# Performance work log

Measured on AMD Instinct MI355X. Metric: run time of the kernel, lower is better.

Reference implementation:

```python
import jax, jax.numpy as jnp
import numpy as np

# --- hash-grid / Field hyperparams (from init_kwargs defaults) ---
L = 16            # n_levels
F = 2             # n_features_per_level
LOG2_T = 19
T = 1 << LOG2_T   # hashmap size per level
NMIN = 16         # base_resolution
MAXRES = 512
SCALE = 1.0
HIDDEN = 32
OUT_DIM = 1
N = 2_000_000
B = float(np.exp(np.log(MAXRES * SCALE / NMIN) / (L - 1)))  # per_level_scale
PRIMES = jnp.array([1, 2654435761, 805459861], dtype=jnp.uint32)
# 8 corner offsets of the unit cube, (8,3)
CORNERS = jnp.array([[(c >> 0) & 1, (c >> 1) & 1, (c >> 2) & 1] for c in range(8)], dtype=jnp.uint32)


def hash_encode(xn, table):
    """xn: (N,3) in [0,1]; table: (L,T,F). Returns (N, L*F)."""
    feats = []
    for l in range(L):  # fixed small loop over levels
        s = NMIN * (B ** l) - 1.0          # tcnn-style grid scale
        pos = xn * s                        # (N,3)
        p0 = jnp.floor(pos)
        w = pos - p0                        # trilinear fracs, (N,3)
        p0i = p0.astype(jnp.uint32)
        corner = p0i[:, None, :] + CORNERS[None, :, :]          # (N,8,3)
        h = corner * PRIMES                                      # (N,8,3) uint32 wrap-mul
        idx = (h[..., 0] ^ h[..., 1] ^ h[..., 2]) & jnp.uint32(T - 1)  # (N,8)
        # trilinear weights per corner: prod over dims of w or (1-w)
        cw = jnp.where(CORNERS[None, :, :] == 1, w[:, None, :], 1.0 - w[:, None, :])
        cw = cw.prod(axis=-1)                                    # (N,8)
        g = table[l][idx.astype(jnp.int32)]                      # (N,8,F)
        feats.append(jnp.einsum('ncf,nc->nf', g, cw))            # (N,F)
    return jnp.concatenate(feats, axis=-1)                       # (N, L*F)


def setup_inputs() -> dict:
    key = jax.random.key(0)
    ks = jax.random.split(key, 8)
    x = jax.random.uniform(ks[0], (N, 3), jnp.float32)  # coords in [0,1) subset of [-scale,scale]
    table = jax.random.normal(ks[1], (L, T, F), jnp.float32) * 1e-2
    W0 = jax.random.normal(ks[2], (L * F + 3, HIDDEN), jnp.float32) * 0.1
    b0 = jnp.zeros((HIDDEN,), jnp.float32)
    W1 = jax.random.normal(ks[3], (HIDDEN, HIDDEN), jnp.float32) * 0.1
    b1 = jnp.zeros((HIDDEN,), jnp.float32)
    Wout = jax.random.normal(ks[4], (HIDDEN, OUT_DIM), jnp.float32) * 0.1
    bout = jnp.zeros((OUT_DIM,), jnp.float32)
    return {"x": x, "table": table, "W0": W0, "b0": b0, "W1": W1, "b1": b1, "Wout": Wout, "bout": bout}


def reference(x, table, W0, b0, W1, b1, Wout, bout):
    # density(): normalize coords to [0,1]
    xn = (x + SCALE) / (2.0 * SCALE)
    # back_prop=0: encoder sees detached coords
    h = hash_encode(jax.lax.stop_gradient(xn), table)   # (N, L*F)
    feat = jnp.concatenate([xn, h], axis=-1)            # (N, 35)  torch.cat([x, h], 1)
    h1 = jax.nn.elu(feat @ W0 + b0)
    h2 = jax.nn.elu(h1 @ W1 + b1)
    out = h2 @ Wout + bout                              # (N, 1)
    return out
```

## Files before the change

kernel.cpp:

```cpp
#include <hip/hip_runtime.h>
#include <hip/hip_fp16.h>
#include <cmath>

#define LVL   16
#define NDENSE 11
#define NHASH  (LVL - NDENSE)
#define TSIZE (1u << 19)
#define TMASK (TSIZE - 1u)
#define HID   32
#define PRIME1 2654435761u
#define PRIME2 805459861u

struct Scales { float s[LVL]; };
struct DenseInfo {
    int X0[NDENSE];
    int dim[NDENSE];
    int dimsq[NDENSE];
    int base[NDENSE];
    int eoff[NDENSE + 1];
};
struct PtInfo {
    int P1[NDENSE];
    int pbase[NDENSE];
    int ptotal;
};

typedef _Float16 f16x8 __attribute__((ext_vector_type(8)));
typedef float    f32x4 __attribute__((ext_vector_type(4)));
typedef float    f32x2 __attribute__((ext_vector_type(2)));
typedef unsigned u32x4 __attribute__((ext_vector_type(4)));

__device__ __forceinline__ float elu_f(float v) {
    return v > 0.0f ? v : __expf(v) - 1.0f;
}
__device__ __forceinline__ unsigned hashed(unsigned cx, unsigned cy, unsigned cz) {
    return (cx ^ (cy * PRIME1) ^ (cz * PRIME2)) & TMASK;
}

__device__ __forceinline__ unsigned enc_pair(float a, float b) {
    return ((unsigned)__builtin_amdgcn_cvt_pk_fp8_f32(a * 64.0f, b * 64.0f, 0, false)) & 0xFFFFu;
}
__device__ __forceinline__ f32x2 dec_lo(unsigned d) {
    return __builtin_amdgcn_cvt_pk_f32_fp8((int)d, false);
}
__device__ __forceinline__ f32x2 dec_hi(unsigned d) {
    return __builtin_amdgcn_cvt_pk_f32_fp8((int)d, true);
}
__device__ __forceinline__ unsigned pack_ff(_Float16 a, _Float16 b) {
    unsigned short ua = __builtin_bit_cast(unsigned short, a);
    unsigned short ub = __builtin_bit_cast(unsigned short, b);
    return (unsigned)ua | ((unsigned)ub << 16);
}
__device__ __forceinline__ unsigned pack_f2(f32x2 f) {
    return pack_ff((_Float16)f.x, (_Float16)f.y);
}

__global__ __launch_bounds__(256)
void convert_hash8(const f32x2* __restrict__ src, unsigned short* __restrict__ dst)
{
    int i = blockIdx.x * blockDim.x + threadIdx.x;
    if (i >= NHASH * (int)TSIZE) return;
    int l = NDENSE + i / (int)TSIZE;
    int s = i & (int)TMASK;
    f32x2 v = src[(size_t)l * TSIZE + s];
    dst[i] = (unsigned short)enc_pair(v.x, v.y);
}

__global__ __launch_bounds__(256)
void dense_pts(const float* __restrict__ table, unsigned short* __restrict__ pts,
               DenseInfo di, PtInfo pi)
{
    int p = blockIdx.x * blockDim.x + threadIdx.x;
    if (p >= pi.ptotal) return;
    int l = 0;
#pragma unroll
    for (int k = 1; k < NDENSE; ++k) if (p >= pi.pbase[k]) l = k;
    int X0 = 0, D1 = 1, pb = 0;
#pragma unroll
    for (int k = 0; k < NDENSE; ++k)
        if (l == k) { X0 = di.X0[k]; D1 = pi.P1[k]; pb = pi.pbase[k]; }
    int lp = p - pb;
    int x = lp % D1; int r = lp / D1;
    int y = r % D1;  int z = r / D1;
    unsigned cx = (unsigned)(X0 + x), cy = (unsigned)(X0 + y), cz = (unsigned)(X0 + z);
    const f32x2* __restrict__ tl = (const f32x2*)table + (size_t)l * TSIZE;
    f32x2 v = tl[hashed(cx, cy, cz)];
    pts[p] = (unsigned short)enc_pair(v.x, v.y);
}

__global__ __launch_bounds__(256)
void dense_cells(const unsigned short* __restrict__ pts, u32x4* __restrict__ dtab,
                 DenseInfo di, PtInfo pi)
{
    int e = blockIdx.x * blockDim.x + threadIdx.x;
    if (e >= di.eoff[NDENSE]) return;
    int l = 0;
#pragma unroll
    for (int k = 1; k < NDENSE; ++k) if (e >= di.eoff[k]) l = k;
    int D = 1, D1 = 1, base = 0, eo = 0, pb = 0;
#pragma unroll
    for (int k = 0; k < NDENSE; ++k)
        if (l == k) { D = di.dim[k]; D1 = pi.P1[k]; base = di.base[k]; eo = di.eoff[k]; pb = pi.pbase[k]; }
    int le = e - eo;
    int ex = le % D; int r = le / D;
    int ey = r % D;  int ez = r / D;
    const unsigned short* __restrict__ q = pts + pb;
    int i00 = ex + (ey + ez * D1) * D1;
    int i01 = i00 + D1;
    int i10 = i00 + D1 * D1;
    int i11 = i10 + D1;
    u32x4 Q;
    Q.x = (unsigned)q[i00] | ((unsigned)q[i00 + 1] << 16);
    Q.y = (unsigned)q[i01] | ((unsigned)q[i01 + 1] << 16);
    Q.z = (unsigned)q[i10] | ((unsigned)q[i10 + 1] << 16);
    Q.w = (unsigned)q[i11] | ((unsigned)q[i11 + 1] << 16);
    dtab[base + le] = Q;
}

__global__ __launch_bounds__(256)
void dense_prep8(const float* __restrict__ table, u32x4* __restrict__ dtab,
                 DenseInfo di)
{
    int e = blockIdx.x * blockDim.x + threadIdx.x;
    if (e >= di.eoff[NDENSE]) return;
    int l = 0;
#pragma unroll
    for (int k = 1; k < NDENSE; ++k) if (e >= di.eoff[k]) l = k;
    int X0 = 0, D = 1, base = 0, eo = 0;
#pragma unroll
    for (int k = 0; k < NDENSE; ++k)
        if (l == k) { X0 = di.X0[k]; D = di.dim[k]; base = di.base[k]; eo = di.eoff[k]; }
    int le = e - eo;
    int ex = le % D; int r = le / D;
    int ey = r % D;  int ez = r / D;
    unsigned cx = (unsigned)(X0 + ex);
    unsigned cy = (unsigned)(X0 + ey);
    unsigned cz = (unsigned)(X0 + ez);
    const f32x2* __restrict__ tl = (const f32x2*)table + (size_t)l * TSIZE;
    f32x2 c0 = tl[hashed(cx,      cy,      cz)];
    f32x2 c1 = tl[hashed(cx + 1u, cy,      cz)];
    f32x2 c2 = tl[hashed(cx,      cy + 1u, cz)];
    f32x2 c3 = tl[hashed(cx + 1u, cy + 1u, cz)];
    f32x2 c4 = tl[hashed(cx,      cy,      cz + 1u)];
    f32x2 c5 = tl[hashed(cx + 1u, cy,      cz + 1u)];
    f32x2 c6 = tl[hashed(cx,      cy + 1u, cz + 1u)];
    f32x2 c7 = tl[hashed(cx + 1u, cy + 1u, cz + 1u)];
    u32x4 Q;
    Q.x = enc_pair(c0.x, c0.y) | (enc_pair(c1.x, c1.y) << 16);
    Q.y = enc_pair(c2.x, c2.y) | (enc_pair(c3.x, c3.y) << 16);
    Q.z = enc_pair(c4.x, c4.y) | (enc_pair(c5.x, c5.y) << 16);
    Q.w = enc_pair(c6.x, c6.y) | (enc_pair(c7.x, c7.y) << 16);
    dtab[base + le] = Q;
}

__global__ void prep_frags(const float* __restrict__ W0, const float* __restrict__ W1,
                           const float* __restrict__ Wout, _Float16* __restrict__ frags)
{
    int idx = blockIdx.x * blockDim.x + threadIdx.x;
    if (idx >= 14*64*8) return;
    int f = idx >> 9;
    int rem = idx & 511;
    int lane = rem >> 3;
    int j = rem & 7;
    int q = lane >> 4;
    int nn = lane & 15;

    float w = 0.0f;
    bool lo;
    if (f < 8) {
        int part = f >> 2, kt = (f >> 1) & 1, nt = f & 1;
        int k = kt*32 + q*8 + j;
        int ncol = nt*16 + nn;
        float val = 0.0f;
        if (k < 32)      val = W0[(3 + k)  * HID + ncol];
        else if (k < 35) val = W0[(k - 32) * HID + ncol];
        else if (k < 38) val = W0[(k - 35) * HID + ncol];
        w = val; lo = (part == 1);
    } else if (f < 12) {
        int part = (f - 8) >> 1, nt = (f - 8) & 1;
        int k = q*8 + j;
        int ncol = nt*16 + nn;
        w = W1[k * HID + ncol]; lo = (part == 1);
    } else {
        int part = f - 12;
        int k = q*8 + j;
        w = (nn == 0) ? Wout[k] : 0.0f; lo = (part == 1);
    }
    _Float16 hi = (_Float16)w;
    frags[idx] = lo ? (_Float16)(w - (float)hi) : hi;
}

struct HL {
    unsigned d0, d1, d2, d3;
    unsigned e0, e1, e2, e3;
    unsigned i0, i1, i2, i3, dm;
    float wx, wy, wz;
};

__device__ __forceinline__ void hash_issue(HL& h, const unsigned* __restrict__ hq,
                                           float xn0, float xn1, float xn2, float s)
{
    float px = xn0 * s, py = xn1 * s, pz = xn2 * s;
    float fx = floorf(px), fy = floorf(py), fz = floorf(pz);
    h.wx = px - fx; h.wy = py - fy; h.wz = pz - fz;
    unsigned x0 = (unsigned)fx, y0 = (unsigned)fy, z0 = (unsigned)fz;
    unsigned hy0 = y0 * PRIME1, hy1 = hy0 + PRIME1;
    unsigned hz0 = z0 * PRIME2, hz1 = hz0 + PRIME2;
    unsigned b00 = hy0 ^ hz0, b10 = hy1 ^ hz0, b01 = hy0 ^ hz1, b11 = hy1 ^ hz1;
    h.i0 = (x0 ^ b00) & TMASK;
    h.i1 = (x0 ^ b10) & TMASK;
    h.i2 = (x0 ^ b01) & TMASK;
    h.i3 = (x0 ^ b11) & TMASK;
    h.dm = (x0 ^ (x0 + 1u)) & TMASK;
    h.d0 = hq[h.i0 >> 1]; h.d1 = hq[h.i1 >> 1];
    h.d2 = hq[h.i2 >> 1]; h.d3 = hq[h.i3 >> 1];
    unsigned j0 = h.i0 ^ h.dm, j1 = h.i1 ^ h.dm, j2 = h.i2 ^ h.dm, j3 = h.i3 ^ h.dm;
    h.e0 = hq[j0 >> 1]; h.e1 = hq[j1 >> 1];
    h.e2 = hq[j2 >> 1]; h.e3 = hq[j3 >> 1];
}

__device__ __forceinline__ unsigned pick_hw(unsigned d, unsigned idx) {
    return (idx & 1u) ? (d >> 16) : (d & 0xFFFFu);
}

__device__ __forceinline__ f32x2 hash_consume(const HL& h)
{
    f32x2 A0 = dec_lo(pick_hw(h.d0, h.i0)), A1 = dec_lo(pick_hw(h.d1, h.i1));
    f32x2 A2 = dec_lo(pick_hw(h.d2, h.i2)), A3 = dec_lo(pick_hw(h.d3, h.i3));
    unsigned j0 = h.i0 ^ h.dm, j1 = h.i1 ^ h.dm, j2 = h.i2 ^ h.dm, j3 = h.i3 ^ h.dm;
    f32x2 C0 = dec_lo(pick_hw(h.e0, j0)), C1 = dec_lo(pick_hw(h.e1, j1));
    f32x2 C2 = dec_lo(pick_hw(h.e2, j2)), C3 = dec_lo(pick_hw(h.e3, j3));
    float uy  = 1.0f - h.wy;
    float uzs = (1.0f - h.wz) * 0.015625f;
    float wzs = h.wz * 0.015625f;
    float w00 = uy * uzs, w10 = h.wy * uzs, w01 = uy * wzs, w11 = h.wy * wzs;
    f32x2 a = A0 * w00 + A1 * w10 + A2 * w01 + A3 * w11;
    f32x2 c = C0 * w00 + C1 * w10 + C2 * w01 + C3 * w11;
    return a * (1.0f - h.wx) + c * h.wx;
}

__global__ __launch_bounds__(256, 4)
void fused_mfma_kernel(const float* __restrict__ x, const unsigned* __restrict__ htab,
                       const u32x4* __restrict__ dtab,
                       const float* __restrict__ b0, const float* __restrict__ b1,
                       const float* __restrict__ bout, const _Float16* __restrict__ fragbuf,
                       float* __restrict__ out, int n, Scales sc, DenseInfo di)
{
    __shared__ __attribute__((aligned(16))) _Float16 featL[256 * 64];
    __shared__ __attribute__((aligned(16))) _Float16 h1h[4][16*32], h1l[4][16*32];

    const int t = threadIdx.x;
    const int pbase = blockIdx.x * 256;
    const int p  = pbase + t;
    const int pc = p < n ? p : n - 1;

    const float xn0 = (x[3*pc+0] + 1.0f) * 0.5f;
    const float xn1 = (x[3*pc+1] + 1.0f) * 0.5f;
    const float xn2 = (x[3*pc+2] + 1.0f) * 0.5f;

    u32x4 qd[NDENSE];
#pragma unroll
    for (int l = 0; l < NDENSE; ++l) {
        const float s = sc.s[l];
        int D = di.dim[l];
        int cx = (int)floorf(xn0 * s) - di.X0[l];
        int cy = (int)floorf(xn1 * s) - di.X0[l];
        int cz = (int)floorf(xn2 * s) - di.X0[l];
        cx = min(max(cx, 0), D - 1);
        cy = min(max(cy, 0), D - 1);
        cz = min(max(cz, 0), D - 1);
        qd[l] = dtab[(size_t)(di.base[l] + cx + cy * D + cz * di.dimsq[l])];
    }

    HL hA, hB, hC;
    hash_issue(hA, htab + 0 * (TSIZE / 2), xn0, xn1, xn2, sc.s[11]);
    hash_issue(hB, htab + 1 * (TSIZE / 2), xn0, xn1, xn2, sc.s[12]);
    hash_issue(hC, htab + 2 * (TSIZE / 2), xn0, xn1, xn2, sc.s[13]);

    unsigned rr[LVL];

#pragma unroll
    for (int l = 0; l < NDENSE; ++l) {
        const float s = sc.s[l];
        float px = xn0 * s, py = xn1 * s, pz = xn2 * s;
        float wx = px - floorf(px), wy = py - floorf(py), wz = pz - floorf(pz);
        u32x4 Q = qd[l];
        f32x2 a00 = dec_lo(Q.x), a10 = dec_hi(Q.x);
        f32x2 a01 = dec_lo(Q.y), a11 = dec_hi(Q.y);
        f32x2 c00 = dec_lo(Q.z), c10 = dec_hi(Q.z);
        f32x2 c01 = dec_lo(Q.w), c11 = dec_hi(Q.w);
        float ux = 1.0f - wx, uy = 1.0f - wy;
        float uzs = (1.0f - wz) * 0.015625f, wzs = wz * 0.015625f;
        f32x2 t0 = a00 * ux + a10 * wx;
        f32x2 t1 = a01 * ux + a11 * wx;
        f32x2 t2 = c00 * ux + c10 * wx;
        f32x2 t3 = c01 * ux + c11 * wx;
        f32x2 u0 = t0 * uy + t1 * wy;
        f32x2 u1 = t2 * uy + t3 * wy;
        f32x2 f  = u0 * uzs + u1 * wzs;
        rr[l] = pack_f2(f);
    }

    rr[11] = pack_f2(hash_consume(hA));
    hash_issue(hA, htab + 3 * (TSIZE / 2), xn0, xn1, xn2, sc.s[14]);
    rr[12] = pack_f2(hash_consume(hB));
    hash_issue(hB, htab + 4 * (TSIZE / 2), xn0, xn1, xn2, sc.s[15]);
    rr[13] = pack_f2(hash_consume(hC));
    rr[14] = pack_f2(hash_consume(hA));
    rr[15] = pack_f2(hash_consume(hB));

    {
        u32x4* fl = (u32x4*)&featL[t * 64];
        const int swt = t & 7;
        u32x4 ch;
        ch.x = rr[0];  ch.y = rr[1];  ch.z = rr[2];  ch.w = rr[3];  fl[0 ^ swt] = ch;
        ch.x = rr[4];  ch.y = rr[5];  ch.z = rr[6];  ch.w = rr[7];  fl[1 ^ swt] = ch;
        ch.x = rr[8];  ch.y = rr[9];  ch.z = rr[10]; ch.w = rr[11]; fl[2 ^ swt] = ch;
        ch.x = rr[12]; ch.y = rr[13]; ch.z = rr[14]; ch.w = rr[15]; fl[3 ^ swt] = ch;
        _Float16 X0h = (_Float16)xn0, X1h = (_Float16)xn1, X2h = (_Float16)xn2;
        _Float16 L0h = (_Float16)(xn0 - (float)X0h);
        _Float16 L1h = (_Float16)(xn1 - (float)X1h);
        _Float16 L2h = (_Float16)(xn2 - (float)X2h);
        ch.x = pack_ff(X0h, X1h); ch.y = pack_ff(X2h, L0h);
        ch.z = pack_ff(L1h, L2h); ch.w = 0;
        fl[4 ^ swt] = ch;
        u32x4 Z; Z.x = 0; Z.y = 0; Z.z = 0; Z.w = 0;
        fl[5 ^ swt] = Z; fl[6 ^ swt] = Z; fl[7 ^ swt] = Z;
    }

    const int lane = t & 63, w = t >> 6;
    const int q = lane >> 4, nn = lane & 15;

    const f16x8* FB = (const f16x8*)fragbuf;
    f16x8 B0h00 = FB[0*64 + lane], B0h01 = FB[1*64 + lane];
    f16x8 B0h10 = FB[2*64 + lane], B0h11 = FB[3*64 + lane];
    f16x8 B0l00 = FB[4*64 + lane], B0l01 = FB[5*64 + lane];
    f16x8 B0l10 = FB[6*64 + lane], B0l11 = FB[7*64 + lane];
    f16x8 B1h0  = FB[8*64 + lane], B1h1  = FB[9*64 + lane];
    f16x8 B1l0  = FB[10*64 + lane], B1l1 = FB[11*64 + lane];
    f16x8 B2h   = FB[12*64 + lane], B2l  = FB[13*64 + lane];

    float bias00 = b0[nn], bias01 = b0[16 + nn];
    float bias10 = b1[nn], bias11 = b1[16 + nn];
    float biasO  = (nn == 0) ? bout[0] : 0.0f;

    _Float16* H1h = &h1h[w][0]; _Float16* H1l = &h1l[w][0];

#pragma unroll
    for (int mt = 0; mt < 4; ++mt) {
        const int mrow = w*64 + mt*16 + nn;
        const f16x8* ar = (const f16x8*)&featL[mrow * 64];
        f16x8 A0 = ar[q ^ (nn & 7)];
        f16x8 A1 = ar[(4 + q) ^ (nn & 7)];

        f32x4 c0 = {bias00, bias00, bias00, bias00};
        f32x4 c1 = {bias01, bias01, bias01, bias01};
        c0 = __builtin_amdgcn_mfma_f32_16x16x32_f16(A0, B0h00, c0, 0, 0, 0);
        c0 = __builtin_amdgcn_mfma_f32_16x16x32_f16(A1, B0h10, c0, 0, 0, 0);
        c0 = __builtin_amdgcn_mfma_f32_16x16x32_f16(A0, B0l00, c0, 0, 0, 0);
        c0 = __builtin_amdgcn_mfma_f32_16x16x32_f16(A1, B0l10, c0, 0, 0, 0);
        c1 = __builtin_amdgcn_mfma_f32_16x16x32_f16(A0, B0h01, c1, 0, 0, 0);
        c1 = __builtin_amdgcn_mfma_f32_16x16x32_f16(A1, B0h11, c1, 0, 0, 0);
        c1 = __builtin_amdgcn_mfma_f32_16x16x32_f16(A0, B0l01, c1, 0, 0, 0);
        c1 = __builtin_amdgcn_mfma_f32_16x16x32_f16(A1, B0l11, c1, 0, 0, 0);

#pragma unroll
        for (int r = 0; r < 4; ++r) {
            int m = q*4 + r;
            float e0 = elu_f(c0[r]);
            _Float16 hh = (_Float16)e0;
            H1h[m*32 + nn]      = hh;
            H1l[m*32 + nn]      = (_Float16)(e0 - (float)hh);
            float e1 = elu_f(c1[r]);
            hh = (_Float16)e1;
            H1h[m*32 + 16 + nn] = hh;
            H1l[m*32 + 16 + nn] = (_Float16)(e1 - (float)hh);
        }

        f16x8 Ah = *(const f16x8*)(H1h + nn*32 + q*8);
        f16x8 Al = *(const f16x8*)(H1l + nn*32 + q*8);
        f32x4 d0 = {bias10, bias10, bias10, bias10};
        f32x4 d1 = {bias11, bias11, bias11, bias11};
        d0 = __builtin_amdgcn_mfma_f32_16x16x32_f16(Ah, B1h0, d0, 0, 0, 0);
        d0 = __builtin_amdgcn_mfma_f32_16x16x32_f16(Ah, B1l0, d0, 0, 0, 0);
        d0 = __builtin_amdgcn_mfma_f32_16x16x32_f16(Al, B1h0, d0, 0, 0, 0);
        d1 = __builtin_amdgcn_mfma_f32_16x16x32_f16(Ah, B1h1, d1, 0, 0, 0);
        d1 = __builtin_amdgcn_mfma_f32_16x16x32_f16(Ah, B1l1, d1, 0, 0, 0);
        d1 = __builtin_amdgcn_mfma_f32_16x16x32_f16(Al, B1h1, d1, 0, 0, 0);

#pragma unroll
        for (int r = 0; r < 4; ++r) {
            int m = q*4 + r;
            float e0 = elu_f(d0[r]);
            _Float16 hh = (_Float16)e0;
            H1h[m*32 + nn]      = hh;
            H1l[m*32 + nn]      = (_Float16)(e0 - (float)hh);
            float e1 = elu_f(d1[r]);
            hh = (_Float16)e1;
            H1h[m*32 + 16 + nn] = hh;
            H1l[m*32 + 16 + nn] = (_Float16)(e1 - (float)hh);
        }

        f16x8 A2h = *(const f16x8*)(H1h + nn*32 + q*8);
        f16x8 A2l = *(const f16x8*)(H1l + nn*32 + q*8);
        f32x4 c3 = {biasO, biasO, biasO, biasO};
        c3 = __builtin_amdgcn_mfma_f32_16x16x32_f16(A2h, B2h, c3, 0, 0, 0);
        c3 = __builtin_amdgcn_mfma_f32_16x16x32_f16(A2h, B2l, c3, 0, 0, 0);
        c3 = __builtin_amdgcn_mfma_f32_16x16x32_f16(A2l, B2h, c3, 0, 0, 0);

        if (nn == 0) {
            int pout = pbase + w*64 + mt*16 + q*4;
#pragma unroll
            for (int r = 0; r < 4; ++r)
                if (pout + r < n) out[pout + r] = c3[r];
        }
    }
}

__device__ __forceinline__ float2 enc_level_f32(float xn0, float xn1, float xn2, float s,
                                                const float2* __restrict__ tb)
{
    float px = xn0 * s, py = xn1 * s, pz = xn2 * s;
    float fx = floorf(px), fy = floorf(py), fz = floorf(pz);
    float wx = px - fx, wy = py - fy, wz = pz - fz;
    unsigned x0 = (unsigned)fx, y0 = (unsigned)fy, z0 = (unsigned)fz;
    unsigned hy0 = y0 * PRIME1, hy1 = hy0 + PRIME1;
    unsigned hz0 = z0 * PRIME2, hz1 = hz0 + PRIME2;
    unsigned b00 = hy0 ^ hz0, b10 = hy1 ^ hz0, b01 = hy0 ^ hz1, b11 = hy1 ^ hz1;
    float2 g000 = tb[( x0       ^ b00) & TMASK];
    float2 g100 = tb[((x0 + 1u) ^ b00) & TMASK];
    float2 g010 = tb[( x0       ^ b10) & TMASK];
    float2 g110 = tb[((x0 + 1u) ^ b10) & TMASK];
    float2 g001 = tb[( x0       ^ b01) & TMASK];
    float2 g101 = tb[((x0 + 1u) ^ b01) & TMASK];
    float2 g011 = tb[( x0       ^ b11) & TMASK];
    float2 g111 = tb[((x0 + 1u) ^ b11) & TMASK];
    float ux = 1.0f - wx, uy = 1.0f - wy, uz = 1.0f - wz;
    float c00 = uy*uz, c10 = wy*uz, c01 = uy*wz, c11 = wy*wz;
    float f0 = ux * (c00*g000.x + c10*g010.x + c01*g001.x + c11*g011.x)
             + wx * (c00*g100.x + c10*g110.x + c01*g101.x + c11*g111.x);
    float f1 = ux * (c00*g000.y + c10*g010.y + c01*g001.y + c11*g011.y)
             + wx * (c00*g100.y + c10*g110.y + c01*g101.y + c11*g111.y);
    return make_float2(f0, f1);
}

__global__ __launch_bounds__(256, 4)
void fused_fp32_kernel(const float* __restrict__ x, const float* __restrict__ table,
                       const float* __restrict__ W0, const float* __restrict__ b0,
                       const float* __restrict__ W1, const float* __restrict__ b1,
                       const float* __restrict__ Wout, const float* __restrict__ bout,
                       float* __restrict__ out, int n, Scales sc)
{
    int tid = blockIdx.x * blockDim.x + threadIdx.x;
    if (tid >= n) return;
    float xn0 = (x[3*tid+0] + 1.0f) * 0.5f;
    float xn1 = (x[3*tid+1] + 1.0f) * 0.5f;
    float xn2 = (x[3*tid+2] + 1.0f) * 0.5f;
    float acc[HID];
#pragma unroll
    for (int j = 0; j < HID; ++j)
        acc[j] = b0[j] + xn0 * W0[0*HID + j] + xn1 * W0[1*HID + j] + xn2 * W0[2*HID + j];
#pragma unroll
    for (int lv = 0; lv < LVL; ++lv) {
        const float2* tb = (const float2*)table + (size_t)lv * TSIZE;
        float2 f = enc_level_f32(xn0, xn1, xn2, sc.s[lv], tb);
        const float* w0r0 = W0 + (3 + 2*lv) * HID;
        const float* w0r1 = W0 + (4 + 2*lv) * HID;
#pragma unroll
        for (int j = 0; j < HID; ++j)
            acc[j] += f.x * w0r0[j] + f.y * w0r1[j];
    }
#pragma unroll
    for (int j = 0; j < HID; ++j) acc[j] = elu_f(acc[j]);
    float acc2[HID];
#pragma unroll
    for (int j = 0; j < HID; ++j) acc2[j] = b1[j];
#pragma unroll
    for (int k = 0; k < HID; ++k) {
        float hk = acc[k];
        const float* w1r = W1 + k * HID;
#pragma unroll
        for (int j = 0; j < HID; ++j) acc2[j] += hk * w1r[j];
    }
    float o = bout[0];
#pragma unroll
    for (int k = 0; k < HID; ++k) o += elu_f(acc2[k]) * Wout[k];
    out[tid] = o;
}

extern "C" void kernel_launch(void* const* d_in, const int* in_sizes, int n_in,
                              void* d_out, int out_size, void* d_ws, size_t ws_size,
                              hipStream_t stream)
{
    const float* x    = (const float*)d_in[0];
    const float* tb   = (const float*)d_in[1];
    const float* W0   = (const float*)d_in[2];
    const float* b0   = (const float*)d_in[3];
    const float* W1   = (const float*)d_in[4];
    const float* b1   = (const float*)d_in[5];
    const float* Wout = (const float*)d_in[6];
    const float* bo   = (const float*)d_in[7];
    float* out = (float*)d_out;

    int n = in_sizes[0] / 3;

    Scales sc;
    DenseInfo di;
    PtInfo pi;
    double B = exp(log(32.0) / 15.0);
    {
        int base = 0, ecum = 0, pcum = 0;
        for (int l = 0; l < LVL; ++l) {
            double sd = 16.0 * pow(B, (double)l) - 1.0;
            sc.s[l] = (float)sd;
            if (l < NDENSE) {
                int X0   = (int)floor(0.5 * sd) - 2; if (X0 < 0) X0 = 0;
                int Xmax = (int)ceil(sd) + 2;
                int dim  = Xmax - X0 + 1;
                di.X0[l] = X0; di.dim[l] = dim; di.dimsq[l] = dim * dim;
                di.base[l] = base; di.eoff[l] = ecum;
                base += dim * dim * dim;
                ecum += dim * dim * dim;
                int D1 = dim + 1;
                pi.P1[l] = D1; pi.pbase[l] = pcum;
                pcum += D1 * D1 * D1;
            }
        }
        di.eoff[NDENSE] = ecum;
        pi.ptotal = pcum;
    }

    const size_t dense_bytes = (size_t)di.eoff[NDENSE] * 16;
    const size_t hash8_bytes = (size_t)NHASH * TSIZE * 2;
    const size_t frag_bytes  = 14 * 64 * 8 * sizeof(_Float16);
    int block = 256;
    int pgrid = (n + block - 1) / block;

    if (ws_size >= dense_bytes + hash8_bytes + frag_bytes) {
        u32x4*          dtab  = (u32x4*)d_ws;
        unsigned short* htab8 = (unsigned short*)((char*)d_ws + dense_bytes);
        _Float16*       frags = (_Float16*)((char*)d_ws + dense_bytes + hash8_bytes);

        int hgrid = (NHASH * (int)TSIZE + block - 1) / block;
        convert_hash8<<<hgrid, block, 0, stream>>>((const f32x2*)tb, htab8);

        if ((size_t)out_size >= (size_t)pi.ptotal * 2) {
            unsigned short* pts = (unsigned short*)d_out;
            int ptg = (pi.ptotal + block - 1) / block;
            dense_pts<<<ptg, block, 0, stream>>>(tb, pts, di, pi);
            int clg = (di.eoff[NDENSE] + block - 1) / block;
            dense_cells<<<clg, block, 0, stream>>>(pts, dtab, di, pi);
        } else {
            int dgrid = (di.eoff[NDENSE] + block - 1) / block;
            dense_prep8<<<dgrid, block, 0, stream>>>(tb, dtab, di);
        }

        prep_frags<<<28, 256, 0, stream>>>(W0, W1, Wout, frags);
        fused_mfma_kernel<<<pgrid, block, 0, stream>>>(x, (const unsigned*)htab8, dtab,
                                                       b0, b1, bo, frags, out, n, sc, di);
    } else {
        fused_fp32_kernel<<<pgrid, block, 0, stream>>>(x, tb, W0, b0, W1, b1, Wout, bo, out, n, sc);
    }
}
```

Before: 626.2 us.

## Read top dense levels from point grid and load hash corners as 16-byte chunks

Only the first 8 dense levels keep per-cell 16-byte corner records. Levels 8-10 now read 8 individual corner values from the per-point fp8 grid, which shrinks the cell table and its build. Hash levels load whole 16-byte chunks, so one load covers both x-corners unless x0 is at a chunk boundary, where a second load is issued. The prep kernels (hash conversion, point grid, weight fragments) are merged into one launch, and pts moves from the output buffer into the workspace. The cost is more scattered 2-byte loads for the top dense levels, plus extra selection logic and register pressure in the main kernel.

```diff
diff --git a/kernel.cpp b/kernel.cpp
--- a/kernel.cpp
+++ b/kernel.cpp
@@ -4,6 +4,7 @@
 
 #define LVL   16
 #define NDENSE 11
+#define NCELL  8
 #define NHASH  (LVL - NDENSE)
 #define TSIZE (1u << 19)
 #define TMASK (TSIZE - 1u)
@@ -15,9 +16,9 @@
 struct DenseInfo {
     int X0[NDENSE];
     int dim[NDENSE];
-    int dimsq[NDENSE];
-    int base[NDENSE];
-    int eoff[NDENSE + 1];
+    int dimsq[NCELL];
+    int cbase[NCELL];
+    int ceoff[NCELL + 1];
 };
 struct PtInfo {
     int P1[NDENSE];
@@ -36,6 +37,11 @@
 __device__ __forceinline__ unsigned hashed(unsigned cx, unsigned cy, unsigned cz) {
     return (cx ^ (cy * PRIME1) ^ (cz * PRIME2)) & TMASK;
 }
+__device__ __forceinline__ unsigned sel4(u32x4 v, unsigned s) {
+    unsigned lo = (s & 1) ? v.y : v.x;
+    unsigned hi = (s & 1) ? v.w : v.z;
+    return (s & 2) ? hi : lo;
+}
 
 __device__ __forceinline__ unsigned enc_pair(float a, float b) {
     return ((unsigned)__builtin_amdgcn_cvt_pk_fp8_f32(a * 64.0f, b * 64.0f, 0, false)) & 0xFFFFu;
@@ -54,38 +60,96 @@
 __device__ __forceinline__ unsigned pack_f2(f32x2 f) {
     return pack_ff((_Float16)f.x, (_Float16)f.y);
 }
+__device__ __forceinline__ unsigned pick_hw(unsigned d, unsigned idx) {
+    return (idx & 1u) ? (d >> 16) : (d & 0xFFFFu);
+}
+
+__device__ __forceinline__ unsigned consume_Q(u32x4 Q, float wx, float wy, float wz)
+{
+    f32x2 a00 = dec_lo(Q.x), a10 = dec_hi(Q.x);
+    f32x2 a01 = dec_lo(Q.y), a11 = dec_hi(Q.y);
+    f32x2 c00 = dec_lo(Q.z), c10 = dec_hi(Q.z);
+    f32x2 c01 = dec_lo(Q.w), c11 = dec_hi(Q.w);
+    float ux = 1.0f - wx, uy = 1.0f - wy;
+    float uzs = (1.0f - wz) * 0.015625f, wzs = wz * 0.015625f;
+    f32x2 t0 = a00 * ux + a10 * wx;
+    f32x2 t1 = a01 * ux + a11 * wx;
+    f32x2 t2 = c00 * ux + c10 * wx;
+    f32x2 t3 = c01 * ux + c11 * wx;
+    f32x2 u0 = t0 * uy + t1 * wy;
+    f32x2 u1 = t2 * uy + t3 * wy;
+    f32x2 f  = u0 * uzs + u1 * wzs;
+    return pack_f2(f);
+}
 
 __global__ __launch_bounds__(256)
-void convert_hash8(const f32x2* __restrict__ src, unsigned short* __restrict__ dst)
-{
+void prep1(const float* __restrict__ table, unsigned short* __restrict__ htab8,
+           unsigned short* __restrict__ pts, const float* __restrict__ W0,
+           const float* __restrict__ W1, const float* __restrict__ Wout,
+           _Float16* __restrict__ frags, DenseInfo di, PtInfo pi)
+{
+    const int NH = NHASH * (int)TSIZE;
     int i = blockIdx.x * blockDim.x + threadIdx.x;
-    if (i >= NHASH * (int)TSIZE) return;
-    int l = NDENSE + i / (int)TSIZE;
-    int s = i & (int)TMASK;
-    f32x2 v = src[(size_t)l * TSIZE + s];
-    dst[i] = (unsigned short)enc_pair(v.x, v.y);
-}
-
-__global__ __launch_bounds__(256)
-void dense_pts(const float* __restrict__ table, unsigned short* __restrict__ pts,
-               DenseInfo di, PtInfo pi)
-{
-    int p = blockIdx.x * blockDim.x + threadIdx.x;
-    if (p >= pi.ptotal) return;
-    int l = 0;
-#pragma unroll
-    for (int k = 1; k < NDENSE; ++k) if (p >= pi.pbase[k]) l = k;
-    int X0 = 0, D1 = 1, pb = 0;
-#pragma unroll
-    for (int k = 0; k < NDENSE; ++k)
-        if (l == k) { X0 = di.X0[k]; D1 = pi.P1[k]; pb = pi.pbase[k]; }
-    int lp = p - pb;
-    int x = lp % D1; int r = lp / D1;
-    int y = r % D1;  int z = r / D1;
-    unsigned cx = (unsigned)(X0 + x), cy = (unsigned)(X0 + y), cz = (unsigned)(X0 + z);
-    const f32x2* __restrict__ tl = (const f32x2*)table + (size_t)l * TSIZE;
-    f32x2 v = tl[hashed(cx, cy, cz)];
-    pts[p] = (unsigned short)enc_pair(v.x, v.y);
+
+    if (i < NH) {
+        int l = NDENSE + i / (int)TSIZE;
+        int s = i & (int)TMASK;
+        const f32x2* src = (const f32x2*)table;
+        f32x2 v = src[(size_t)l * TSIZE + s];
+        htab8[i] = (unsigned short)enc_pair(v.x, v.y);
+        return;
+    }
+    i -= NH;
+    if (i < pi.ptotal) {
+        int l = 0;
+#pragma unroll
+        for (int k = 1; k < NDENSE; ++k) if (i >= pi.pbase[k]) l = k;
+        int X0 = 0, D1 = 1, pb = 0;
+#pragma unroll
+        for (int k = 0; k < NDENSE; ++k)
+            if (l == k) { X0 = di.X0[k]; D1 = pi.P1[k]; pb = pi.pbase[k]; }
+        int lp = i - pb;
+        int x = lp % D1; int r = lp / D1;
+        int y = r % D1;  int z = r / D1;
+        unsigned cx = (unsigned)(X0 + x), cy = (unsigned)(X0 + y), cz = (unsigned)(X0 + z);
+        const f32x2* tl = (const f32x2*)table + (size_t)l * TSIZE;
+        f32x2 v = tl[hashed(cx, cy, cz)];
+        pts[i] = (unsigned short)enc_pair(v.x, v.y);
+        return;
+    }
+    i -= pi.ptotal;
+    if (i >= 14*64*8) return;
+    {
+        int f = i >> 9;
+        int rem = i & 511;
+        int lane = rem >> 3;
+        int j = rem & 7;
+        int q = lane >> 4;
+        int nn = lane & 15;
+        float w = 0.0f;
+        bool lo;
+        if (f < 8) {
+            int part = f >> 2, kt = (f >> 1) & 1, nt = f & 1;
+            int k = kt*32 + q*8 + j;
+            int ncol = nt*16 + nn;
+            float val = 0.0f;
+            if (k < 32)      val = W0[(3 + k)  * HID + ncol];
+            else if (k < 35) val = W0[(k - 32) * HID + ncol];
+            else if (k < 38) val = W0[(k - 35) * HID + ncol];
+            w = val; lo = (part == 1);
+        } else if (f < 12) {
+            int part = (f - 8) >> 1, nt = (f - 8) & 1;
+            int k = q*8 + j;
+            int ncol = nt*16 + nn;
+            w = W1[k * HID + ncol]; lo = (part == 1);
+        } else {
+            int part = f - 12;
+            int k = q*8 + j;
+            w = (nn == 0) ? Wout[k] : 0.0f; lo = (part == 1);
+        }
+        _Float16 hi = (_Float16)w;
+        frags[i] = lo ? (_Float16)(w - (float)hi) : hi;
+    }
 }
 
 __global__ __launch_bounds__(256)
@@ -93,14 +157,14 @@
                  DenseInfo di, PtInfo pi)
 {
     int e = blockIdx.x * blockDim.x + threadIdx.x;
-    if (e >= di.eoff[NDENSE]) return;
+    if (e >= di.ceoff[NCELL]) return;
     int l = 0;
 #pragma unroll
-    for (int k = 1; k < NDENSE; ++k) if (e >= di.eoff[k]) l = k;
+    for (int k = 1; k < NCELL; ++k) if (e >= di.ceoff[k]) l = k;
     int D = 1, D1 = 1, base = 0, eo = 0, pb = 0;
 #pragma unroll
-    for (int k = 0; k < NDENSE; ++k)
-        if (l == k) { D = di.dim[k]; D1 = pi.P1[k]; base = di.base[k]; eo = di.eoff[k]; pb = pi.pbase[k]; }
+    for (int k = 0; k < NCELL; ++k)
+        if (l == k) { D = di.dim[k]; D1 = pi.P1[k]; base = di.cbase[k]; eo = di.ceoff[k]; pb = pi.pbase[k]; }
     int le = e - eo;
     int ex = le % D; int r = le / D;
     int ey = r % D;  int ez = r / D;
@@ -117,134 +181,12 @@
     dtab[base + le] = Q;
 }
 
-__global__ __launch_bounds__(256)
-void dense_prep8(const float* __restrict__ table, u32x4* __restrict__ dtab,
-                 DenseInfo di)
-{
-    int e = blockIdx.x * blockDim.x + threadIdx.x;
-    if (e >= di.eoff[NDENSE]) return;
-    int l = 0;
-#pragma unroll
-    for (int k = 1; k < NDENSE; ++k) if (e >= di.eoff[k]) l = k;
-    int X0 = 0, D = 1, base = 0, eo = 0;
-#pragma unroll
-    for (int k = 0; k < NDENSE; ++k)
-        if (l == k) { X0 = di.X0[k]; D = di.dim[k]; base = di.base[k]; eo = di.eoff[k]; }
-    int le = e - eo;
-    int ex = le % D; int r = le / D;
-    int ey = r % D;  int ez = r / D;
-    unsigned cx = (unsigned)(X0 + ex);
-    unsigned cy = (unsigned)(X0 + ey);
-    unsigned cz = (unsigned)(X0 + ez);
-    const f32x2* __restrict__ tl = (const f32x2*)table + (size_t)l * TSIZE;
-    f32x2 c0 = tl[hashed(cx,      cy,      cz)];
-    f32x2 c1 = tl[hashed(cx + 1u, cy,      cz)];
-    f32x2 c2 = tl[hashed(cx,      cy + 1u, cz)];
-    f32x2 c3 = tl[hashed(cx + 1u, cy + 1u, cz)];
-    f32x2 c4 = tl[hashed(cx,      cy,      cz + 1u)];
-    f32x2 c5 = tl[hashed(cx + 1u, cy,      cz + 1u)];
-    f32x2 c6 = tl[hashed(cx,      cy + 1u, cz + 1u)];
-    f32x2 c7 = tl[hashed(cx + 1u, cy + 1u, cz + 1u)];
-    u32x4 Q;
-    Q.x = enc_pair(c0.x, c0.y) | (enc_pair(c1.x, c1.y) << 16);
-    Q.y = enc_pair(c2.x, c2.y) | (enc_pair(c3.x, c3.y) << 16);
-    Q.z = enc_pair(c4.x, c4.y) | (enc_pair(c5.x, c5.y) << 16);
-    Q.w = enc_pair(c6.x, c6.y) | (enc_pair(c7.x, c7.y) << 16);
-    dtab[base + le] = Q;
-}
-
-__global__ void prep_frags(const float* __restrict__ W0, const float* __restrict__ W1,
-                           const float* __restrict__ Wout, _Float16* __restrict__ frags)
-{
-    int idx = blockIdx.x * blockDim.x + threadIdx.x;
-    if (idx >= 14*64*8) return;
-    int f = idx >> 9;
-    int rem = idx & 511;
-    int lane = rem >> 3;
-    int j = rem & 7;
-    int q = lane >> 4;
-    int nn = lane & 15;
-
-    float w = 0.0f;
-    bool lo;
-    if (f < 8) {
-        int part = f >> 2, kt = (f >> 1) & 1, nt = f & 1;
-        int k = kt*32 + q*8 + j;
-        int ncol = nt*16 + nn;
-        float val = 0.0f;
-        if (k < 32)      val = W0[(3 + k)  * HID + ncol];
-        else if (k < 35) val = W0[(k - 32) * HID + ncol];
-        else if (k < 38) val = W0[(k - 35) * HID + ncol];
-        w = val; lo = (part == 1);
-    } else if (f < 12) {
-        int part = (f - 8) >> 1, nt = (f - 8) & 1;
-        int k = q*8 + j;
-        int ncol = nt*16 + nn;
-        w = W1[k * HID + ncol]; lo = (part == 1);
-    } else {
-        int part = f - 12;
-        int k = q*8 + j;
-        w = (nn == 0) ? Wout[k] : 0.0f; lo = (part == 1);
-    }
-    _Float16 hi = (_Float16)w;
-    frags[idx] = lo ? (_Float16)(w - (float)hi) : hi;
-}
-
-struct HL {
-    unsigned d0, d1, d2, d3;
-    unsigned e0, e1, e2, e3;
-    unsigned i0, i1, i2, i3, dm;
-    float wx, wy, wz;
-};
-
-__device__ __forceinline__ void hash_issue(HL& h, const unsigned* __restrict__ hq,
-                                           float xn0, float xn1, float xn2, float s)
-{
-    float px = xn0 * s, py = xn1 * s, pz = xn2 * s;
-    float fx = floorf(px), fy = floorf(py), fz = floorf(pz);
-    h.wx = px - fx; h.wy = py - fy; h.wz = pz - fz;
-    unsigned x0 = (unsigned)fx, y0 = (unsigned)fy, z0 = (unsigned)fz;
-    unsigned hy0 = y0 * PRIME1, hy1 = hy0 + PRIME1;
-    unsigned hz0 = z0 * PRIME2, hz1 = hz0 + PRIME2;
-    unsigned b00 = hy0 ^ hz0, b10 = hy1 ^ hz0, b01 = hy0 ^ hz1, b11 = hy1 ^ hz1;
-    h.i0 = (x0 ^ b00) & TMASK;
-    h.i1 = (x0 ^ b10) & TMASK;
-    h.i2 = (x0 ^ b01) & TMASK;
-    h.i3 = (x0 ^ b11) & TMASK;
-    h.dm = (x0 ^ (x0 + 1u)) & TMASK;
-    h.d0 = hq[h.i0 >> 1]; h.d1 = hq[h.i1 >> 1];
-    h.d2 = hq[h.i2 >> 1]; h.d3 = hq[h.i3 >> 1];
-    unsigned j0 = h.i0 ^ h.dm, j1 = h.i1 ^ h.dm, j2 = h.i2 ^ h.dm, j3 = h.i3 ^ h.dm;
-    h.e0 = hq[j0 >> 1]; h.e1 = hq[j1 >> 1];
-    h.e2 = hq[j2 >> 1]; h.e3 = hq[j3 >> 1];
-}
-
-__device__ __forceinline__ unsigned pick_hw(unsigned d, unsigned idx) {
-    return (idx & 1u) ? (d >> 16) : (d & 0xFFFFu);
-}
-
-__device__ __forceinline__ f32x2 hash_consume(const HL& h)
-{
-    f32x2 A0 = dec_lo(pick_hw(h.d0, h.i0)), A1 = dec_lo(pick_hw(h.d1, h.i1));
-    f32x2 A2 = dec_lo(pick_hw(h.d2, h.i2)), A3 = dec_lo(pick_hw(h.d3, h.i3));
-    unsigned j0 = h.i0 ^ h.dm, j1 = h.i1 ^ h.dm, j2 = h.i2 ^ h.dm, j3 = h.i3 ^ h.dm;
-    f32x2 C0 = dec_lo(pick_hw(h.e0, j0)), C1 = dec_lo(pick_hw(h.e1, j1));
-    f32x2 C2 = dec_lo(pick_hw(h.e2, j2)), C3 = dec_lo(pick_hw(h.e3, j3));
-    float uy  = 1.0f - h.wy;
-    float uzs = (1.0f - h.wz) * 0.015625f;
-    float wzs = h.wz * 0.015625f;
-    float w00 = uy * uzs, w10 = h.wy * uzs, w01 = uy * wzs, w11 = h.wy * wzs;
-    f32x2 a = A0 * w00 + A1 * w10 + A2 * w01 + A3 * w11;
-    f32x2 c = C0 * w00 + C1 * w10 + C2 * w01 + C3 * w11;
-    return a * (1.0f - h.wx) + c * h.wx;
-}
-
 __global__ __launch_bounds__(256, 4)
-void fused_mfma_kernel(const float* __restrict__ x, const unsigned* __restrict__ htab,
-                       const u32x4* __restrict__ dtab,
+void fused_mfma_kernel(const float* __restrict__ x, const u32x4* __restrict__ htabq,
+                       const u32x4* __restrict__ dtab, const unsigned short* __restrict__ pts,
                        const float* __restrict__ b0, const float* __restrict__ b1,
                        const float* __restrict__ bout, const _Float16* __restrict__ fragbuf,
-                       float* __restrict__ out, int n, Scales sc, DenseInfo di)
+                       float* __restrict__ out, int n, Scales sc, DenseInfo di, PtInfo pi)
 {
     __shared__ __attribute__((aligned(16))) _Float16 featL[256 * 64];
     __shared__ __attribute__((aligned(16))) _Float16 h1h[4][16*32], h1l[4][16*32];
@@ -258,9 +200,10 @@
     const float xn1 = (x[3*pc+1] + 1.0f) * 0.5f;
     const float xn2 = (x[3*pc+2] + 1.0f) * 0.5f;
 
-    u32x4 qd[NDENSE];
-#pragma unroll
-    for (int l = 0; l < NDENSE; ++l) {
+    unsigned pu[3][8];
+#pragma unroll
+    for (int k = 0; k < 3; ++k) {
+        const int l = NCELL + k;
         const float s = sc.s[l];
         int D = di.dim[l];
         int cx = (int)floorf(xn0 * s) - di.X0[l];
@@ -269,45 +212,110 @@
         cx = min(max(cx, 0), D - 1);
         cy = min(max(cy, 0), D - 1);
         cz = min(max(cz, 0), D - 1);
-        qd[l] = dtab[(size_t)(di.base[l] + cx + cy * D + cz * di.dimsq[l])];
-    }
-
-    HL hA, hB, hC;
-    hash_issue(hA, htab + 0 * (TSIZE / 2), xn0, xn1, xn2, sc.s[11]);
-    hash_issue(hB, htab + 1 * (TSIZE / 2), xn0, xn1, xn2, sc.s[12]);
-    hash_issue(hC, htab + 2 * (TSIZE / 2), xn0, xn1, xn2, sc.s[13]);
+        const int P1 = pi.P1[l];
+        const unsigned short* __restrict__ pl = pts + pi.pbase[l];
+        int i00 = cx + P1 * (cy + P1 * cz);
+        int i1  = i00 + P1 * P1;
+        pu[k][0] = pl[i00];          pu[k][1] = pl[i00 + 1];
+        pu[k][2] = pl[i00 + P1];     pu[k][3] = pl[i00 + P1 + 1];
+        pu[k][4] = pl[i1];           pu[k][5] = pl[i1 + 1];
+        pu[k][6] = pl[i1 + P1];      pu[k][7] = pl[i1 + P1 + 1];
+    }
+
+    u32x4 qd[NCELL];
+#pragma unroll
+    for (int l = 0; l < NCELL; ++l) {
+        const float s = sc.s[l];
+        int D = di.dim[l];
+        int cx = (int)floorf(xn0 * s) - di.X0[l];
+        int cy = (int)floorf(xn1 * s) - di.X0[l];
+        int cz = (int)floorf(xn2 * s) - di.X0[l];
+        cx = min(max(cx, 0), D - 1);
+        cy = min(max(cy, 0), D - 1);
+        cz = min(max(cz, 0), D - 1);
+        qd[l] = dtab[(size_t)(di.cbase[l] + cx + cy * D + cz * di.dimsq[l])];
+    }
 
     unsigned rr[LVL];
 
 #pragma unroll
-    for (int l = 0; l < NDENSE; ++l) {
+    for (int l = NDENSE; l < LVL; ++l) {
+        const u32x4* __restrict__ qt = htabq + ((size_t)(l - NDENSE) * TSIZE >> 3);
+        const float s = sc.s[l];
+        float px = xn0 * s, py = xn1 * s, pz = xn2 * s;
+        float fx = floorf(px), fy = floorf(py), fz = floorf(pz);
+        float wx = px - fx, wy = py - fy, wz = pz - fz;
+        unsigned x0 = (unsigned)fx, y0 = (unsigned)fy, z0 = (unsigned)fz;
+        unsigned hy0 = y0 * PRIME1, hy1 = hy0 + PRIME1;
+        unsigned hz0 = z0 * PRIME2, hz1 = hz0 + PRIME2;
+        unsigned b00 = hy0 ^ hz0, b10 = hy1 ^ hz0, b01 = hy0 ^ hz1, b11 = hy1 ^ hz1;
+        unsigned i0 = (x0 ^ b00) & TMASK;
+        unsigned i1 = (x0 ^ b10) & TMASK;
+        unsigned i2 = (x0 ^ b01) & TMASK;
+        unsigned i3 = (x0 ^ b11) & TMASK;
+
+        u32x4 Q0 = qt[i0 >> 3];
+        u32x4 Q1 = qt[i1 >> 3];
+        u32x4 Q2 = qt[i2 >> 3];
+        u32x4 Q3 = qt[i3 >> 3];
+
+        unsigned dm = (x0 ^ (x0 + 1u)) & TMASK;
+        unsigned j0 = i0 ^ dm, j1 = i1 ^ dm, j2 = i2 ^ dm, j3 = i3 ^ dm;
+
+        unsigned hc0, hc1, hc2, hc3;
+        if ((x0 & 7u) == 7u) {
+            u32x4 R0 = qt[j0 >> 3];
+            u32x4 R1 = qt[j1 >> 3];
+            u32x4 R2 = qt[j2 >> 3];
+            u32x4 R3 = qt[j3 >> 3];
+            hc0 = pick_hw(sel4(R0, (j0 >> 1) & 3), j0);
+            hc1 = pick_hw(sel4(R1, (j1 >> 1) & 3), j1);
+            hc2 = pick_hw(sel4(R2, (j2 >> 1) & 3), j2);
+            hc3 = pick_hw(sel4(R3, (j3 >> 1) & 3), j3);
+        } else {
+            hc0 = pick_hw(sel4(Q0, (j0 >> 1) & 3), j0);
+            hc1 = pick_hw(sel4(Q1, (j1 >> 1) & 3), j1);
+            hc2 = pick_hw(sel4(Q2, (j2 >> 1) & 3), j2);
+            hc3 = pick_hw(sel4(Q3, (j3 >> 1) & 3), j3);
+        }
+        unsigned ha0 = pick_hw(sel4(Q0, (i0 >> 1) & 3), i0);
+        unsigned ha1 = pick_hw(sel4(Q1, (i1 >> 1) & 3), i1);
+        unsigned ha2 = pick_hw(sel4(Q2, (i2 >> 1) & 3), i2);
+        unsigned ha3 = pick_hw(sel4(Q3, (i3 >> 1) & 3), i3);
+
+        f32x2 A0 = dec_lo(ha0), A1 = dec_lo(ha1), A2 = dec_lo(ha2), A3 = dec_lo(ha3);
+        f32x2 C0 = dec_lo(hc0), C1 = dec_lo(hc1), C2 = dec_lo(hc2), C3 = dec_lo(hc3);
+        float uy  = 1.0f - wy;
+        float uzs = (1.0f - wz) * 0.015625f;
+        float wzs = wz * 0.015625f;
+        float w00 = uy * uzs, w10 = wy * uzs, w01 = uy * wzs, w11 = wy * wzs;
+        f32x2 a = A0 * w00 + A1 * w10 + A2 * w01 + A3 * w11;
+        f32x2 c = C0 * w00 + C1 * w10 + C2 * w01 + C3 * w11;
+        f32x2 f = a * (1.0f - wx) + c * wx;
+        rr[l] = pack_f2(f);
+    }
+
+#pragma unroll
+    for (int l = 0; l < NCELL; ++l) {
         const float s = sc.s[l];
         float px = xn0 * s, py = xn1 * s, pz = xn2 * s;
         float wx = px - floorf(px), wy = py - floorf(py), wz = pz - floorf(pz);
-        u32x4 Q = qd[l];
-        f32x2 a00 = dec_lo(Q.x), a10 = dec_hi(Q.x);
-        f32x2 a01 = dec_lo(Q.y), a11 = dec_hi(Q.y);
-        f32x2 c00 = dec_lo(Q.z), c10 = dec_hi(Q.z);
-        f32x2 c01 = dec_lo(Q.w), c11 = dec_hi(Q.w);
-        float ux = 1.0f - wx, uy = 1.0f - wy;
-        float uzs = (1.0f - wz) * 0.015625f, wzs = wz * 0.015625f;
-        f32x2 t0 = a00 * ux + a10 * wx;
-        f32x2 t1 = a01 * ux + a11 * wx;
-        f32x2 t2 = c00 * ux + c10 * wx;
-        f32x2 t3 = c01 * ux + c11 * wx;
-        f32x2 u0 = t0 * uy + t1 * wy;
-        f32x2 u1 = t2 * uy + t3 * wy;
-        f32x2 f  = u0 * uzs + u1 * wzs;
-        rr[l] = pack_f2(f);
-    }
-
-    rr[11] = pack_f2(hash_consume(hA));
-    hash_issue(hA, htab + 3 * (TSIZE / 2), xn0, xn1, xn2, sc.s[14]);
-    rr[12] = pack_f2(hash_consume(hB));
-    hash_issue(hB, htab + 4 * (TSIZE / 2), xn0, xn1, xn2, sc.s[15]);
-    rr[13] = pack_f2(hash_consume(hC));
-    rr[14] = pack_f2(hash_consume(hA));
-    rr[15] = pack_f2(hash_consume(hB));
+        rr[l] = consume_Q(qd[l], wx, wy, wz);
+    }
+
+#pragma unroll
+    for (int k = 0; k < 3; ++k) {
+        const int l = NCELL + k;
+        const float s = sc.s[l];
+        float px = xn0 * s, py = xn1 * s, pz = xn2 * s;
+        float wx = px - floorf(px), wy = py - floorf(py), wz = pz - floorf(pz);
+        u32x4 Q;
+        Q.x = pu[k][0] | (pu[k][1] << 16);
+        Q.y = pu[k][2] | (pu[k][3] << 16);
+        Q.z = pu[k][4] | (pu[k][5] << 16);
+        Q.w = pu[k][6] | (pu[k][7] << 16);
+        rr[l] = consume_Q(Q, wx, wy, wz);
+    }
 
     {
         u32x4* fl = (u32x4*)&featL[t * 64];
@@ -509,7 +517,7 @@
     PtInfo pi;
     double B = exp(log(32.0) / 15.0);
     {
-        int base = 0, ecum = 0, pcum = 0;
+        int cbase = 0, ccum = 0, pcum = 0;
         for (int l = 0; l < LVL; ++l) {
             double sd = 16.0 * pow(B, (double)l) - 1.0;
             sc.s[l] = (float)sd;
@@ -517,47 +525,45 @@
                 int X0   = (int)floor(0.5 * sd) - 2; if (X0 < 0) X0 = 0;
                 int Xmax = (int)ceil(sd) + 2;
                 int dim  = Xmax - X0 + 1;
-                di.X0[l] = X0; di.dim[l] = dim; di.dimsq[l] = dim * dim;
-                di.base[l] = base; di.eoff[l] = ecum;
-                base += dim * dim * dim;
-                ecum += dim * dim * dim;
+                di.X0[l] = X0; di.dim[l] = dim;
                 int D1 = dim + 1;
                 pi.P1[l] = D1; pi.pbase[l] = pcum;
                 pcum += D1 * D1 * D1;
+                if (l < NCELL) {
+                    di.dimsq[l] = dim * dim;
+                    di.cbase[l] = cbase; di.ceoff[l] = ccum;
+                    cbase += dim * dim * dim;
+                    ccum  += dim * dim * dim;
+                }
             }
         }
-        di.eoff[NDENSE] = ecum;
+        di.ceoff[NCELL] = ccum;
         pi.ptotal = pcum;
     }
 
-    const size_t dense_bytes = (size_t)di.eoff[NDENSE] * 16;
-    const size_t hash8_bytes = (size_t)NHASH * TSIZE * 2;
+    auto align256 = [](size_t v) { return (v + 255) & ~(size_t)255; };
+    const size_t cells_bytes = align256((size_t)di.ceoff[NCELL] * 16);
+    const size_t hash8_bytes = align256((size_t)NHASH * TSIZE * 2);
+    const size_t pts_bytes   = align256((size_t)pi.ptotal * 2);
     const size_t frag_bytes  = 14 * 64 * 8 * sizeof(_Float16);
     int block = 256;
     int pgrid = (n + block - 1) / block;
 
-    if (ws_size >= dense_bytes + hash8_bytes + frag_bytes) {
+    if (ws_size >= cells_bytes + hash8_bytes + pts_bytes + frag_bytes) {
         u32x4*          dtab  = (u32x4*)d_ws;
-        unsigned short* htab8 = (unsigned short*)((char*)d_ws + dense_bytes);
-        _Float16*       frags = (_Float16*)((char*)d_ws + dense_bytes + hash8_bytes);
-
-        int hgrid = (NHASH * (int)TSIZE + block - 1) / block;
-        convert_hash8<<<hgrid, block, 0, stream>>>((const f32x2*)tb, htab8);
-
-        if ((size_t)out_size >= (size_t)pi.ptotal * 2) {
-            unsigned short* pts = (unsigned short*)d_out;
-            int ptg = (pi.ptotal + block - 1) / block;
-            dense_pts<<<ptg, block, 0, stream>>>(tb, pts, di, pi);
-            int clg = (di.eoff[NDENSE] + block - 1) / block;
-            dense_cells<<<clg, block, 0, stream>>>(pts, dtab, di, pi);
-        } else {
-            int dgrid = (di.eoff[NDENSE] + block - 1) / block;
-            dense_prep8<<<dgrid, block, 0, stream>>>(tb, dtab, di);
-        }
-
-        prep_frags<<<28, 256, 0, stream>>>(W0, W1, Wout, frags);
-        fused_mfma_kernel<<<pgrid, block, 0, stream>>>(x, (const unsigned*)htab8, dtab,
-                                                       b0, b1, bo, frags, out, n, sc, di);
+        unsigned short* htab8 = (unsigned short*)((char*)d_ws + cells_bytes);
+        unsigned short* pts   = (unsigned short*)((char*)d_ws + cells_bytes + hash8_bytes);
+        _Float16*       frags = (_Float16*)((char*)d_ws + cells_bytes + hash8_bytes + pts_bytes);
+
+        int work1 = NHASH * (int)TSIZE + pi.ptotal + 14*64*8;
+        int g1 = (work1 + block - 1) / block;
+        prep1<<<g1, block, 0, stream>>>(tb, htab8, pts, W0, W1, Wout, frags, di, pi);
+
+        int g2 = (di.ceoff[NCELL] + block - 1) / block;
+        dense_cells<<<g2, block, 0, stream>>>(pts, dtab, di, pi);
+
+        fused_mfma_kernel<<<pgrid, block, 0, stream>>>(x, (const u32x4*)htab8, dtab, pts,
+                                                       b0, b1, bo, frags, out, n, sc, di, pi);
     } else {
         fused_fp32_kernel<<<pgrid, block, 0, stream>>>(x, tb, W0, b0, W1, b1, Wout, bo, out, n, sc);
     }
```

Result: slower. 841.3 us (+34.3%).
